# Kernel tuning notes

Measured on AMD Instinct MI355X. Metric: run time of the kernel, lower is better.

Reference implementation:

```python
import jax, jax.numpy as jnp
import numpy as np
import math

N_EMB = 256
N_HEAD = 8
B_SEGS = 128
T_SEG = 256  # equal-length segments; N = B_SEGS * T_SEG


def setup_inputs() -> dict:
    key = jax.random.key(0)
    ks = jax.random.split(key, 10)
    N = B_SEGS * T_SEG
    x = jax.random.normal(ks[0], (N, N_EMB), dtype=jnp.float32)
    batch = jnp.repeat(jnp.arange(B_SEGS, dtype=jnp.int64), T_SEG)
    s = 1.0 / math.sqrt(N_EMB)
    def lin(k):
        kw, kb = jax.random.split(k)
        W = jax.random.uniform(kw, (N_EMB, N_EMB), jnp.float32, -s, s)
        b = jax.random.uniform(kb, (N_EMB,), jnp.float32, -s, s)
        return W, b
    Wq, bq = lin(ks[1])
    Wk, bk = lin(ks[2])
    Wv, bv = lin(ks[3])
    Wp, bp = lin(ks[4])
    return {"x": x, "batch": batch, "Wq": Wq, "bq": bq, "Wk": Wk, "bk": bk,
            "Wv": Wv, "bv": bv, "Wp": Wp, "bp": bp}


def reference(x, batch, Wq, bq, Wk, bk, Wv, bv, Wp, bp):
    # Dropout layers are identity in eval / p=0.
    N, C = x.shape
    H = N_HEAD
    hd = C // H
    B = int(batch[-1]) + 1        # equal-length segments
    T = N // B
    xr = x.reshape(B, T, C)
    # per-segment QKV projections: [B,H,T,hd]
    def heads(W, b):
        return (xr @ W.T + b).reshape(B, T, H, hd).transpose(0, 2, 1, 3)
    q = heads(Wq, bq)
    k = heads(Wk, bk)
    v = heads(Wv, bv)
    scores = jnp.einsum('bhtd,bhsd->bhts', q, k) * (1.0 / math.sqrt(hd))
    attn = jax.nn.softmax(scores, axis=-1)          # [B,H,T,T]
    y = jnp.einsum('bhts,bhsd->bhtd', attn, v)      # [B,H,T,hd]
    y = y.transpose(0, 2, 1, 3).reshape(B, T, C)
    y = y @ Wp.T + bp
    attn_mean = attn.mean(axis=1)                   # head-mean per segment [B,T,T]
    return y.reshape(N, C), attn_mean
```

## Files before the change

kernel.cpp:

```cpp
#include <hip/hip_runtime.h>
#include <hip/hip_bf16.h>
#include <stdint.h>

typedef unsigned short u16;
typedef __bf16 bf16_t;
typedef bf16_t bf16x8 __attribute__((ext_vector_type(8)));
typedef float f32x4 __attribute__((ext_vector_type(4)));

#define NTOK 32768
#define CEMB 256
#define NHEAD 8
#define HD 32
#define BSEG 128
#define TSEG 256

#define SCQ (0.17677669529663687f * 1.4426950408889634f)

static __device__ __forceinline__ bf16x8 ld16(const u16* p) {
  uint4 v = *reinterpret_cast<const uint4*>(p);
  return __builtin_bit_cast(bf16x8, v);
}
static __device__ __forceinline__ u16 f2b(float f) {
  return __builtin_bit_cast(u16, (bf16_t)f);
}

typedef __attribute__((address_space(1))) const void GASV;
typedef __attribute__((address_space(3))) void LASV;
static __device__ __forceinline__ void stage16(const u16* g, u16* l) {
  __builtin_amdgcn_global_load_lds((GASV*)g, (LASV*)l, 16, 0, 0);
}

__global__ void k_convert(const float* __restrict__ x,
                          const float* __restrict__ wq, const float* __restrict__ wk,
                          const float* __restrict__ wv, const float* __restrict__ wp,
                          u16* __restrict__ xb, u16* __restrict__ wb) {
  const int XSLOTS = (NTOK * CEMB) / 8;
  const int WSLOTS = (4 * CEMB * CEMB) / 8;
  int slot = blockIdx.x * blockDim.x + threadIdx.x;
  if (slot >= XSLOTS + WSLOTS) return;
  const float* src;
  u16* dst;
  if (slot < XSLOTS) {
    src = x + slot * 8;
    dst = xb + slot * 8;
  } else {
    int e = (slot - XSLOTS) * 8;
    int wsel = e >> 16, off = e & 65535;
    const float* s0 = (wsel == 0) ? wq : ((wsel == 1) ? wk : ((wsel == 2) ? wv : wp));
    src = s0 + off;
    dst = wb + e;
  }
  float4 a = reinterpret_cast<const float4*>(src)[0];
  float4 b = reinterpret_cast<const float4*>(src)[1];
  u16 o[8] = {f2b(a.x), f2b(a.y), f2b(a.z), f2b(a.w),
              f2b(b.x), f2b(b.y), f2b(b.z), f2b(b.w)};
  *reinterpret_cast<uint4*>(dst) = *reinterpret_cast<const uint4*>(o);
}

#define GEMM_MAIN_LOOP(Asrc, Bsrc)                                              \
  f32x4 acc[4][4];                                                              \
  _Pragma("unroll") for (int mf = 0; mf < 4; ++mf)                              \
      _Pragma("unroll") for (int nf = 0; nf < 4; ++nf) {                        \
    f32x4 z = {0.f, 0.f, 0.f, 0.f};                                             \
    acc[mf][nf] = z;                                                            \
  }                                                                             \
  u16* As = lds;                                                                \
  u16* Bs = lds + 16384;                                                        \
  auto STAGE = [&](int buf, int kt) {                                           \
    _Pragma("unroll") for (int i = 0; i < 4; ++i) {                             \
      int cidx = i * 256 + tid;                                                 \
      int row = cidx >> 3;                                                      \
      int scb = ((cidx & 7) << 4) ^ ((row & 7) << 4);        \
      u16* dst_lds = As + buf * 8192 + (i * 256 + w * 64) * 8;                  \
      stage16(Asrc + (size_t)(m0 + row) * CEMB + kt * 64 + (scb >> 1), dst_lds);\
      u16* dst_ldsb = Bs + buf * 8192 + (i * 256 + w * 64) * 8;                 \
      stage16(Bsrc + (size_t)(n0 + row) * CEMB + kt * 64 + (scb >> 1), dst_ldsb);\
    }                                                                           \
  };                                                                            \
  STAGE(0, 0);                                                                  \
  __syncthreads();                                                              \
  for (int kt = 0; kt < 4; ++kt) {                                              \
    int buf = kt & 1;                                                           \
    if (kt < 3) STAGE(buf ^ 1, kt + 1);                                         \
    bf16x8 av[4][2], bw[4][2];                                                  \
    _Pragma("unroll") for (int mf = 0; mf < 4; ++mf)                            \
        _Pragma("unroll") for (int kk = 0; kk < 2; ++kk) {                      \
      int row = wr * 64 + mf * 16 + lr;                                         \
      int byte = row * 128 + ((kk * 64 + lg * 16) ^ ((row & 7) << 4));          \
      av[mf][kk] = *reinterpret_cast<const bf16x8*>(                            \
          (const char*)(As + buf * 8192) + byte);                               \
    }                                                                           \
    _Pragma("unroll") for (int nf = 0; nf < 4; ++nf)                            \
        _Pragma("unroll") for (int kk = 0; kk < 2; ++kk) {                      \
      int row = wc * 64 + nf * 16 + lr;                                         \
      int byte = row * 128 + ((kk * 64 + lg * 16) ^ ((row & 7) << 4));          \
      bw[nf][kk] = *reinterpret_cast<const bf16x8*>(                            \
          (const char*)(Bs + buf * 8192) + byte);                               \
    }                                                                           \
    _Pragma("unroll") for (int kk = 0; kk < 2; ++kk)                            \
        _Pragma("unroll") for (int nf = 0; nf < 4; ++nf)                        \
            _Pragma("unroll") for (int mf = 0; mf < 4; ++mf)                    \
      acc[mf][nf] = __builtin_amdgcn_mfma_f32_16x16x32_bf16(                    \
          av[mf][kk], bw[nf][kk], acc[mf][nf], 0, 0, 0);                        \
    __syncthreads();                                                            \
  }

__global__ __launch_bounds__(256, 2)
void k_qkv(const u16* __restrict__ xb, const u16* __restrict__ wb,
           const float* __restrict__ bq, const float* __restrict__ bk,
           const float* __restrict__ bv,
           u16* __restrict__ q_ws, u16* __restrict__ k_ws, u16* __restrict__ v_ws) {
  const int d = blockIdx.x;
  const int xcd = d & 7, i = d >> 3;
  const int m_idx = xcd * 32 + i / 6;
  const int rr = i % 6;
  const int mode = rr >> 1;
  const int n0 = (rr & 1) * 128;
  const int m0 = m_idx * 128;
  const int tid = threadIdx.x;
  const int w = tid >> 6, l = tid & 63;
  const int lr = l & 15, lg = l >> 4;
  const int wr = w >> 1, wc = w & 1;

  __shared__ u16 lds[32768];

  const u16* W = wb + mode * (CEMB * CEMB);
  const float* bias = (mode == 0) ? bq : ((mode == 1) ? bk : bv);

  GEMM_MAIN_LOOP(xb, W)

  float bb[4];
#pragma unroll
  for (int nf = 0; nf < 4; ++nf) bb[nf] = bias[n0 + wc * 64 + nf * 16 + lr];

  const float osc = (mode == 0) ? SCQ : 1.0f;

  if (mode < 2) {
    u16* Et = lds;
#pragma unroll
    for (int mf = 0; mf < 4; ++mf)
#pragma unroll
      for (int nf = 0; nf < 4; ++nf)
#pragma unroll
        for (int r = 0; r < 4; ++r) {
          int row = wr * 64 + mf * 16 + lg * 4 + r;
          int col = wc * 64 + nf * 16 + lr;
          int byte = (row * 256 + col * 2) ^ ((row & 7) << 4);
          *(u16*)((char*)Et + byte) = f2b((acc[mf][nf][r] + bb[nf]) * osc);
        }
    __syncthreads();
    u16* out = (mode == 0) ? q_ws : k_ws;
    int row_l = tid >> 1, half = tid & 1;
    u16* dstp = out + (size_t)(m0 + row_l) * CEMB + n0 + half * 64;
#pragma unroll
    for (int j = 0; j < 8; ++j) {
      int byte = row_l * 256 + (((half * 64 + j * 8) * 2) ^ ((row_l & 7) << 4));
      *reinterpret_cast<uint4*>(dstp + j * 8) =
          *reinterpret_cast<const uint4*>((const char*)Et + byte);
    }
  } else {
    u16* Vt = lds;
#pragma unroll
    for (int mf = 0; mf < 4; ++mf)
#pragma unroll
      for (int nf = 0; nf < 4; ++nf)
#pragma unroll
        for (int r = 0; r < 4; ++r) {
          int row = wr * 64 + mf * 16 + lg * 4 + r;
          int col = wc * 64 + nf * 16 + lr;
          int byte = (col * 256 + row * 2) ^ ((col & 7) << 4);
          *(u16*)((char*)Vt + byte) = f2b(acc[mf][nf][r] + bb[nf]);
        }
    __syncthreads();
    int col_l = tid >> 1, half = tid & 1;
    int c = n0 + col_l, hh = c >> 5, dd = c & 31;
    int bs = m0 >> 8, t0 = m0 & 255;
    u16* dst = v_ws + ((size_t)(bs * NHEAD + hh) * HD + dd) * TSEG + t0 + half * 64;
#pragma unroll
    for (int j = 0; j < 8; ++j) {
      int byte = col_l * 256 + ((half * 128 + j * 16) ^ ((col_l & 7) << 4));
      *reinterpret_cast<uint4*>(dst + j * 8) =
          *reinterpret_cast<const uint4*>((const char*)Vt + byte);
    }
  }
}

__global__ __launch_bounds__(1024, 4)
void k_attn(const u16* __restrict__ q_ws, const u16* __restrict__ k_ws,
            const u16* __restrict__ v_ws,
            u16* __restrict__ y_ws, float* __restrict__ mean_out) {
  const int dblk = blockIdx.x;
  const int xcd = dblk & 7, ii = dblk >> 3;
  const int b = xcd * 16 + (ii >> 1);
  const int th = ii & 1;
  const int tid = threadIdx.x;
  const int w = tid >> 6, l = tid & 63;
  const int lr = l & 15, lg = l >> 4;
  const int wt = w & 7, sh = w >> 3;
  const int tbase = th * 128 + wt * 16;

  extern __shared__ u16 ldsKV[];
  float* smb = reinterpret_cast<float*>(ldsKV + 32768);
  float* ylds = reinterpret_cast<float*>(ldsKV + 33280);

  float macc[8][4];
#pragma unroll
  for (int st = 0; st < 8; ++st)
#pragma unroll
    for (int r = 0; r < 4; ++r) macc[st][r] = 0.f;

  const u16* qseg = q_ws + (size_t)b * TSEG * CEMB;
  const u16* kseg = k_ws + (size_t)b * TSEG * CEMB;
  const u16* vseg = v_ws + (size_t)(b * NHEAD) * HD * TSEG;

  auto STAGE_KV = [&](int hn, int bn) {
    int idx = tid;
    int c = idx >> 6, l2 = idx & 63;
    int lr2 = l2 & 15, lg2 = l2 >> 4;
    int srow = 32 * (c >> 1) + 4 * (c & 1) + 8 * (lr2 >> 2) + (lr2 & 3);
    stage16(kseg + srow * CEMB + hn * HD + lg2 * 8, ldsKV + (bn * 1024 + idx) * 8);
    int vrow = (c >> 3) * 16 + lr2;
    int vcol = (c & 7) * 32 + lg2 * 8;
    stage16(vseg + (size_t)(hn * HD + vrow) * TSEG + vcol,
            ldsKV + 16384 + (bn * 1024 + idx) * 8);
  };

  STAGE_KV(0, 0);
  bf16x8 qf = ld16(qseg + (tbase + lr) * CEMB + lg * 8);

  const int own_slot = wt * 2 + sh;
  const int par_slot = wt * 2 + (1 - sh);

  for (int h = 0; h < NHEAD; ++h) {
    const int bn = h & 1;
    __syncthreads();
    if (h < 7) STAGE_KV(h + 1, bn ^ 1);
    const u16* Kb = ldsKV + bn * 8192;
    const u16* Vb = ldsKV + 16384 + bn * 8192;

    float s[8][4];
#pragma unroll
    for (int st = 0; st < 8; ++st) {
      bf16x8 kf = *reinterpret_cast<const bf16x8*>(Kb + ((sh * 8 + st) * 64 + l) * 8);
      f32x4 z = {0.f, 0.f, 0.f, 0.f};
      f32x4 dd = __builtin_amdgcn_mfma_f32_16x16x32_bf16(kf, qf, z, 0, 0, 0);
#pragma unroll
      for (int r = 0; r < 4; ++r) s[st][r] = dd[r];
    }

    qf = ld16(qseg + (tbase + lr) * CEMB + ((h + 1) & 7) * HD + lg * 8);

    float s0 = 0.f, s1 = 0.f, s2 = 0.f, s3 = 0.f;
#pragma unroll
    for (int st = 0; st < 8; ++st) {
      float p0 = exp2f(s[st][0]);
      float p1 = exp2f(s[st][1]);
      float p2 = exp2f(s[st][2]);
      float p3 = exp2f(s[st][3]);
      s[st][0] = p0; s[st][1] = p1; s[st][2] = p2; s[st][3] = p3;
      s0 += p0; s1 += p1; s2 += p2; s3 += p3;
    }
    float sm = (s0 + s1) + (s2 + s3);
    sm += __shfl_xor(sm, 16, 64);
    sm += __shfl_xor(sm, 32, 64);

    bf16x8 pb[4];
#pragma unroll
    for (int kk = 0; kk < 4; ++kk)
#pragma unroll
      for (int e = 0; e < 4; ++e) {
        pb[kk][e] = (bf16_t)s[2 * kk][e];
        pb[kk][4 + e] = (bf16_t)s[2 * kk + 1][e];
      }

    f32x4 y0 = {0.f, 0.f, 0.f, 0.f}, y1 = {0.f, 0.f, 0.f, 0.f};
#pragma unroll
    for (int kk = 0; kk < 4; ++kk) {
      bf16x8 vf0 = *reinterpret_cast<const bf16x8*>(Vb + ((0 * 8 + sh * 4 + kk) * 64 + l) * 8);
      bf16x8 vf1 = *reinterpret_cast<const bf16x8*>(Vb + ((1 * 8 + sh * 4 + kk) * 64 + l) * 8);
      y0 = __builtin_amdgcn_mfma_f32_16x16x32_bf16(vf0, pb[kk], y0, 0, 0, 0);
      y1 = __builtin_amdgcn_mfma_f32_16x16x32_bf16(vf1, pb[kk], y1, 0, 0, 0);
    }

    if (l < 16) smb[own_slot * 16 + l] = sm;
    {
      f32x4 ywr = (sh == 0) ? y1 : y0;
      *reinterpret_cast<f32x4*>(ylds + own_slot * 272 + lg * 68 + lr * 4) = ywr;
    }

    __builtin_amdgcn_sched_barrier(0);
    asm volatile("s_waitcnt lgkmcnt(0)" ::: "memory");
    __builtin_amdgcn_s_barrier();
    __builtin_amdgcn_sched_barrier(0);

    float smT = sm + smb[par_slot * 16 + lr];
    float inv = __builtin_amdgcn_rcpf(smT);

#pragma unroll
    for (int st = 0; st < 8; ++st)
#pragma unroll
      for (int r = 0; r < 4; ++r)
        macc[st][r] = fmaf(s[st][r], inv, macc[st][r]);

    {
      f32x4 ymine = (sh == 0) ? y0 : y1;
      f32x4 ypar = *reinterpret_cast<const f32x4*>(ylds + par_slot * 272 + lg * 68 + lr * 4);
      u16 o[4];
#pragma unroll
      for (int r = 0; r < 4; ++r) o[r] = f2b((ymine[r] + ypar[r]) * inv);
      *reinterpret_cast<uint2*>(
          y_ws + (size_t)(b * TSEG + tbase + lr) * CEMB + h * HD + sh * 16 + lg * 4) =
          *reinterpret_cast<const uint2*>(o);
    }
  }

  __syncthreads();

  float* smem = reinterpret_cast<float*>(ldsKV);
  float* smw = smem + w * (16 * 65) + lr * 65;
  const int trow = l >> 2;
  const int cql = (l & 3) * 4;
  const float* srcp = smem + w * (16 * 65) + trow * 65 + cql;
  float* gdst = mean_out + (size_t)(b * TSEG + tbase + trow) * TSEG + sh * 128 + cql;

  for (int c = 0; c < 2; ++c) {
#pragma unroll
    for (int j = 0; j < 4; ++j) {
      int st = 4 * c + j;
      int sl = 32 * ((st >> 1) & 1) + 4 * (st & 1) + 8 * lg;
#pragma unroll
      for (int r = 0; r < 4; ++r) smw[sl + r] = macc[st][r] * 0.125f;
    }
#pragma unroll
    for (int j = 0; j < 4; ++j)
      *reinterpret_cast<f32x4*>(gdst + c * 64 + j * 16) =
          *reinterpret_cast<const f32x4*>(srcp + j * 16);
  }
}

__global__ __launch_bounds__(256, 2)
void k_proj(const u16* __restrict__ yb, const u16* __restrict__ wb,
            const float* __restrict__ bp, float* __restrict__ out) {
  const int d = blockIdx.x;
  const int xcd = d & 7, i = d >> 3;
  const int m0 = (xcd * 32 + (i >> 1)) * 128;
  const int n0 = (i & 1) * 128;
  const int tid = threadIdx.x;
  const int w = tid >> 6, l = tid & 63;
  const int lr = l & 15, lg = l >> 4;
  const int wr = w >> 1, wc = w & 1;
  const u16* W = wb + 3 * (CEMB * CEMB);

  __shared__ u16 lds[32768];

  GEMM_MAIN_LOOP(yb, W)

  float bb[4];
#pragma unroll
  for (int nf = 0; nf < 4; ++nf) bb[nf] = bp[n0 + wc * 64 + nf * 16 + lr];
#pragma unroll
  for (int mf = 0; mf < 4; ++mf)
#pragma unroll
    for (int nf = 0; nf < 4; ++nf)
#pragma unroll
      for (int r = 0; r < 4; ++r) {
        int m = m0 + wr * 64 + mf * 16 + lg * 4 + r;
        int c = n0 + wc * 64 + nf * 16 + lr;
        out[(size_t)m * CEMB + c] = acc[mf][nf][r] + bb[nf];
      }
}

extern "C" void kernel_launch(void* const* d_in, const int* in_sizes, int n_in,
                              void* d_out, int out_size, void* d_ws, size_t ws_size,
                              hipStream_t stream) {
  (void)in_sizes; (void)n_in; (void)out_size; (void)ws_size;
  const float* x  = (const float*)d_in[0];
  const float* Wq = (const float*)d_in[2];
  const float* bq = (const float*)d_in[3];
  const float* Wk = (const float*)d_in[4];
  const float* bk = (const float*)d_in[5];
  const float* Wv = (const float*)d_in[6];
  const float* bv = (const float*)d_in[7];
  const float* Wp = (const float*)d_in[8];
  const float* bp = (const float*)d_in[9];
  float* out = (float*)d_out;

  char* ws = (char*)d_ws;
  u16* xb   = (u16*)(ws);
  u16* wb   = (u16*)(ws + 16777216);
  u16* q_ws = (u16*)(ws + 17301504);
  u16* k_ws = (u16*)(ws + 34078720);
  u16* v_ws = (u16*)(ws + 50855936);
  u16* y_ws = xb;
  float* mean_out = out + (size_t)NTOK * CEMB;

  k_convert<<<4224, 256, 0, stream>>>(x, Wq, Wk, Wv, Wp, xb, wb);
  k_qkv<<<1536, 256, 0, stream>>>(xb, wb, bq, bk, bv, q_ws, k_ws, v_ws);
  k_attn<<<256, 1024, 83968, stream>>>(q_ws, k_ws, v_ws, y_ws, mean_out);
  k_proj<<<512, 256, 0, stream>>>(y_ws, wb, bp, out);
}
```

Baseline: 88.68 us.

## Fuse output projection into attention kernel via LDS-resident Y tile

The attention kernel now keeps its 128x256 bf16 output tile in a swizzled LDS region instead of writing it to global memory. After the head-mean store, it runs the Wp projection GEMM directly, double-buffering Wp k-slices in LDS, and writes the final fp32 output with bias. This removes the separate projection launch and the global round trip of the Y intermediate. In exchange, dynamic LDS grows to about 146 KB per block, and the projection is serialized at the tail of each attention block.

Result: faster. 84.60 us (-4.6%).

```diff
diff --git a/kernel.cpp b/kernel.cpp
--- a/kernel.cpp
+++ b/kernel.cpp
@@ -187,8 +187,9 @@
 
 __global__ __launch_bounds__(1024, 4)
 void k_attn(const u16* __restrict__ q_ws, const u16* __restrict__ k_ws,
-            const u16* __restrict__ v_ws,
-            u16* __restrict__ y_ws, float* __restrict__ mean_out) {
+            const u16* __restrict__ v_ws, const u16* __restrict__ wb,
+            const float* __restrict__ bp,
+            float* __restrict__ out, float* __restrict__ mean_out) {
   const int dblk = blockIdx.x;
   const int xcd = dblk & 7, ii = dblk >> 3;
   const int b = xcd * 16 + (ii >> 1);
@@ -202,6 +203,7 @@
   extern __shared__ u16 ldsKV[];
   float* smb = reinterpret_cast<float*>(ldsKV + 32768);
   float* ylds = reinterpret_cast<float*>(ldsKV + 33280);
+  char* yTile = reinterpret_cast<char*>(ldsKV) + 83968;
 
   float macc[8][4];
 #pragma unroll
@@ -308,66 +310,111 @@
       u16 o[4];
 #pragma unroll
       for (int r = 0; r < 4; ++r) o[r] = f2b((ymine[r] + ypar[r]) * inv);
-      *reinterpret_cast<uint2*>(
-          y_ws + (size_t)(b * TSEG + tbase + lr) * CEMB + h * HD + sh * 16 + lg * 4) =
+      int row = wt * 16 + lr;
+      int colb = h * 64 + sh * 32 + lg * 8;
+      *reinterpret_cast<uint2*>(yTile + row * 512 + (colb ^ ((row & 7) << 4))) =
           *reinterpret_cast<const uint2*>(o);
     }
   }
 
   __syncthreads();
 
-  float* smem = reinterpret_cast<float*>(ldsKV);
-  float* smw = smem + w * (16 * 65) + lr * 65;
-  const int trow = l >> 2;
-  const int cql = (l & 3) * 4;
-  const float* srcp = smem + w * (16 * 65) + trow * 65 + cql;
-  float* gdst = mean_out + (size_t)(b * TSEG + tbase + trow) * TSEG + sh * 128 + cql;
-
-  for (int c = 0; c < 2; ++c) {
-#pragma unroll
-    for (int j = 0; j < 4; ++j) {
-      int st = 4 * c + j;
-      int sl = 32 * ((st >> 1) & 1) + 4 * (st & 1) + 8 * lg;
-#pragma unroll
-      for (int r = 0; r < 4; ++r) smw[sl + r] = macc[st][r] * 0.125f;
-    }
-#pragma unroll
-    for (int j = 0; j < 4; ++j)
-      *reinterpret_cast<f32x4*>(gdst + c * 64 + j * 16) =
-          *reinterpret_cast<const f32x4*>(srcp + j * 16);
-  }
-}
-
-__global__ __launch_bounds__(256, 2)
-void k_proj(const u16* __restrict__ yb, const u16* __restrict__ wb,
-            const float* __restrict__ bp, float* __restrict__ out) {
-  const int d = blockIdx.x;
-  const int xcd = d & 7, i = d >> 3;
-  const int m0 = (xcd * 32 + (i >> 1)) * 128;
-  const int n0 = (i & 1) * 128;
-  const int tid = threadIdx.x;
-  const int w = tid >> 6, l = tid & 63;
-  const int lr = l & 15, lg = l >> 4;
-  const int wr = w >> 1, wc = w & 1;
-  const u16* W = wb + 3 * (CEMB * CEMB);
-
-  __shared__ u16 lds[32768];
-
-  GEMM_MAIN_LOOP(yb, W)
-
-  float bb[4];
-#pragma unroll
-  for (int nf = 0; nf < 4; ++nf) bb[nf] = bp[n0 + wc * 64 + nf * 16 + lr];
-#pragma unroll
-  for (int mf = 0; mf < 4; ++mf)
-#pragma unroll
-    for (int nf = 0; nf < 4; ++nf)
-#pragma unroll
-      for (int r = 0; r < 4; ++r) {
-        int m = m0 + wr * 64 + mf * 16 + lg * 4 + r;
-        int c = n0 + wc * 64 + nf * 16 + lr;
-        out[(size_t)m * CEMB + c] = acc[mf][nf][r] + bb[nf];
+  {
+    float* smem = reinterpret_cast<float*>(ldsKV);
+    float* smw = smem + w * (16 * 65) + lr * 65;
+    const int trow = l >> 2;
+    const int cql = (l & 3) * 4;
+    const float* srcp = smem + w * (16 * 65) + trow * 65 + cql;
+    float* gdst = mean_out + (size_t)(b * TSEG + tbase + trow) * TSEG + sh * 128 + cql;
+    for (int c = 0; c < 2; ++c) {
+#pragma unroll
+      for (int j = 0; j < 4; ++j) {
+        int st = 4 * c + j;
+        int sl = 32 * ((st >> 1) & 1) + 4 * (st & 1) + 8 * lg;
+#pragma unroll
+        for (int r = 0; r < 4; ++r) smw[sl + r] = macc[st][r] * 0.125f;
       }
+#pragma unroll
+      for (int j = 0; j < 4; ++j)
+        *reinterpret_cast<f32x4*>(gdst + c * 64 + j * 16) =
+            *reinterpret_cast<const f32x4*>(srcp + j * 16);
+    }
+  }
+  __syncthreads();
+
+  {
+    const u16* wbP = wb + 3 * (CEMB * CEMB);
+    const int wrP = w >> 2, wcP = w & 3;
+
+    auto STAGE_W = [&](int kt, int bn) {
+      u16* Wb = ldsKV + bn * 16384;
+#pragma unroll
+      for (int r = 0; r < 2; ++r) {
+        int cidx = (r * 16 + w) * 64 + l;
+        int row = cidx >> 3;
+        int scb = ((cidx & 7) << 4) ^ ((row & 7) << 4);
+        stage16(wbP + (size_t)row * CEMB + kt * 64 + (scb >> 1),
+                Wb + (r * 16 + w) * 512);
+      }
+    };
+
+    f32x4 acc[2][4];
+#pragma unroll
+    for (int mf = 0; mf < 2; ++mf)
+#pragma unroll
+      for (int nf = 0; nf < 4; ++nf) {
+        f32x4 z = {0.f, 0.f, 0.f, 0.f};
+        acc[mf][nf] = z;
+      }
+
+    STAGE_W(0, 0);
+    __syncthreads();
+    for (int kt = 0; kt < 4; ++kt) {
+      int buf = kt & 1;
+      if (kt < 3) STAGE_W(kt + 1, buf ^ 1);
+      const char* Wb = (const char*)(ldsKV + buf * 16384);
+      bf16x8 av[2][2], bw[4][2];
+#pragma unroll
+      for (int mf = 0; mf < 2; ++mf)
+#pragma unroll
+        for (int kk = 0; kk < 2; ++kk) {
+          int row = wrP * 32 + mf * 16 + lr;
+          int byte = row * 512 + ((kt * 128 + kk * 64 + lg * 16) ^ ((row & 7) << 4));
+          av[mf][kk] = *reinterpret_cast<const bf16x8*>(yTile + byte);
+        }
+#pragma unroll
+      for (int nf = 0; nf < 4; ++nf)
+#pragma unroll
+        for (int kk = 0; kk < 2; ++kk) {
+          int row = wcP * 64 + nf * 16 + lr;
+          int byte = row * 128 + ((kk * 64 + lg * 16) ^ ((row & 7) << 4));
+          bw[nf][kk] = *reinterpret_cast<const bf16x8*>(Wb + byte);
+        }
+#pragma unroll
+      for (int kk = 0; kk < 2; ++kk)
+#pragma unroll
+        for (int nf = 0; nf < 4; ++nf)
+#pragma unroll
+          for (int mf = 0; mf < 2; ++mf)
+            acc[mf][nf] = __builtin_amdgcn_mfma_f32_16x16x32_bf16(
+                av[mf][kk], bw[nf][kk], acc[mf][nf], 0, 0, 0);
+      __syncthreads();
+    }
+
+    float bb[4];
+#pragma unroll
+    for (int nf = 0; nf < 4; ++nf) bb[nf] = bp[wcP * 64 + nf * 16 + lr];
+#pragma unroll
+    for (int mf = 0; mf < 2; ++mf)
+#pragma unroll
+      for (int nf = 0; nf < 4; ++nf)
+#pragma unroll
+        for (int r = 0; r < 4; ++r) {
+          int m = b * TSEG + th * 128 + wrP * 32 + mf * 16 + lg * 4 + r;
+          int c = wcP * 64 + nf * 16 + lr;
+          out[(size_t)m * CEMB + c] = acc[mf][nf][r] + bb[nf];
+        }
+  }
 }
 
 extern "C" void kernel_launch(void* const* d_in, const int* in_sizes, int n_in,
@@ -391,11 +438,9 @@
   u16* q_ws = (u16*)(ws + 17301504);
   u16* k_ws = (u16*)(ws + 34078720);
   u16* v_ws = (u16*)(ws + 50855936);
-  u16* y_ws = xb;
   float* mean_out = out + (size_t)NTOK * CEMB;
 
   k_convert<<<4224, 256, 0, stream>>>(x, Wq, Wk, Wv, Wp, xb, wb);
   k_qkv<<<1536, 256, 0, stream>>>(xb, wb, bq, bk, bv, q_ws, k_ws, v_ws);
-  k_attn<<<256, 1024, 83968, stream>>>(q_ws, k_ws, v_ws, y_ws, mean_out);
-  k_proj<<<512, 256, 0, stream>>>(y_ws, wb, bp, out);
-}
+  k_attn<<<256, 1024, 149504, stream>>>(q_ws, k_ws, v_ws, wb, bp, out, mean_out);
+}
```
